# Kernel tuning notes

Hardware: AMD Instinct MI355X
Metric: run time of the kernel (lower is better)

Reference implementation:

```python
import jax, jax.numpy as jnp
import numpy as np

N_NODES = 50000
N_EDGES = 800000
EPS = 1e-12


def _l2norm(x):
    # F.normalize(x, p=2, dim=1)
    n = jnp.sqrt(jnp.sum(x * x, axis=1, keepdims=True))
    return x / jnp.maximum(n, EPS)


def _sage_layer(h, src, dst, inv_deg, W_self, W_neigh, b, last):
    # mean aggregation over in-neighbors: gather src feats, scatter-add to dst
    msg = jax.ops.segment_sum(h[src], dst, num_segments=N_NODES)  # [N, d]
    h_neigh = msg * inv_deg  # [N, d]
    rst = h @ W_self + h_neigh @ W_neigh + b
    if not last:
        rst = jax.nn.relu(rst)
        rst = _l2norm(rst)
    return rst


def setup_inputs() -> dict:
    key = jax.random.key(0)
    ks = jax.random.split(key, 10)
    d_in, d_h, d_out = 128, 128, 64
    s = lambda k, sh, fan: jax.random.normal(k, sh, jnp.float32) / np.sqrt(fan)
    return {
        "features": jax.random.normal(ks[0], (N_NODES, d_in), jnp.float32),
        "src": jax.random.randint(ks[1], (N_EDGES,), 0, N_NODES, jnp.int32),
        "dst": jax.random.randint(ks[2], (N_EDGES,), 0, N_NODES, jnp.int32),
        "W_self0": s(ks[3], (d_in, d_h), d_in),
        "W_neigh0": s(ks[4], (d_in, d_h), d_in),
        "b0": jnp.zeros((d_h,), jnp.float32),
        "W_self1": s(ks[5], (d_h, d_h), d_h),
        "W_neigh1": s(ks[6], (d_h, d_h), d_h),
        "b1": jnp.zeros((d_h,), jnp.float32),
        "W_self2": s(ks[7], (d_h, d_out), d_h),
        "W_neigh2": s(ks[8], (d_h, d_out), d_h),
        "b2": jnp.zeros((d_out,), jnp.float32),
    }


def reference(features, src, dst, W_self0, W_neigh0, b0, W_self1, W_neigh1, b1, W_self2, W_neigh2, b2):
    # in-degree for mean aggregation (clamped to avoid div-by-zero)
    deg = jax.ops.segment_sum(jnp.ones((N_EDGES,), jnp.float32), dst, num_segments=N_NODES)
    inv_deg = (1.0 / jnp.maximum(deg, 1.0))[:, None]  # [N,1]
    h = _sage_layer(features, src, dst, inv_deg, W_self0, W_neigh0, b0, last=False)
    h = _sage_layer(h, src, dst, inv_deg, W_self1, W_neigh1, b1, last=False)
    out = _sage_layer(h, src, dst, inv_deg, W_self2, W_neigh2, b2, last=True)
    return out
```

## Files before the change

kernel.cpp:

```cpp
#include <hip/hip_runtime.h>
#include <hip/hip_bf16.h>

#define N_NODES 50000
#define N_EDGES 800000
#define NBUCKET 196
#define NPB 256
#define BUCKET_CAP 7168
#define PART_EDGES 4096
#define PART_BLOCKS ((N_EDGES + PART_EDGES - 1) / PART_EDGES)
#define SENTINEL 0xFFFFFFFFu

typedef __attribute__((ext_vector_type(8))) short bf16x8;
typedef __attribute__((ext_vector_type(4))) float f32x4;

__device__ __forceinline__ float bf2f(unsigned short u) {
    unsigned int x = ((unsigned int)u) << 16;
    return __uint_as_float(x);
}
__device__ __forceinline__ unsigned short f2bf(float f) {
    unsigned int x = __float_as_uint(f);
    unsigned int lsb = (x >> 16) & 1u;
    x += 0x7fffu + lsb;
    return (unsigned short)(x >> 16);
}

#define NF2 ((N_NODES * 64 + 255) / 256)
__global__ __launch_bounds__(256) void k_prep(
        const float* __restrict__ Ws0, const float* __restrict__ Wn0,
        const float* __restrict__ Ws1, const float* __restrict__ Wn1,
        const float* __restrict__ Ws2, const float* __restrict__ Wn2,
        __hip_bfloat16* __restrict__ frag0, __hip_bfloat16* __restrict__ frag1,
        __hip_bfloat16* __restrict__ frag2,
        const float2* __restrict__ fin, unsigned int* __restrict__ fout,
        int* __restrict__ cursor, int* __restrict__ valid) {
    int b = blockIdx.x;
    if (b >= 40 + NF2) {
        int tid = threadIdx.x;
        if (tid < NBUCKET) { cursor[tid] = 0; valid[tid] = 0; }
        return;
    }
    if (b >= 40) {
        int i = (b - 40) * 256 + threadIdx.x;
        if (i < N_NODES * 64) {
            float2 v = fin[i];
            fout[i] = ((unsigned int)f2bf(v.y) << 16) | (unsigned int)f2bf(v.x);
        }
        return;
    }
    const float* Wself;
    const float* Wneigh;
    __hip_bfloat16* frag;
    int Dout, lb;
    if (b < 16)      { Wself = Ws0; Wneigh = Wn0; frag = frag0; Dout = 128; lb = b; }
    else if (b < 32) { Wself = Ws1; Wneigh = Wn1; frag = frag1; Dout = 128; lb = b - 16; }
    else             { Wself = Ws2; Wneigh = Wn2; frag = frag2; Dout = 64;  lb = b - 32; }
    int t = lb * 256 + threadIdx.x;
    int nCt = Dout >> 4;
    int total = nCt * 8 * 64;
    if (t >= total) return;
    int lane = t & 63;
    int kt = (t >> 6) & 7;
    int ct = t >> 9;
    int q = lane >> 4;
    int n = ct * 16 + (lane & 15);
    unsigned short* dstp = (unsigned short*)frag + ((size_t)((ct * 8 + kt) * 64 + lane)) * 8;
    #pragma unroll
    for (int j = 0; j < 8; ++j) {
        int k = kt * 32 + q * 8 + j;
        float v = (k < 128) ? Wself[k * Dout + n] : Wneigh[(k - 128) * Dout + n];
        dstp[j] = f2bf(v);
    }
}

__global__ __launch_bounds__(256) void k_partA(const int* __restrict__ src,
                                               const int* __restrict__ dst,
                                               int* __restrict__ cursor,
                                               int* __restrict__ valid,
                                               unsigned int* __restrict__ bucketArr) {
    __shared__ int hist[NBUCKET];
    __shared__ int base[NBUCKET];
    __shared__ int cnt[NBUCKET];
    int tid = threadIdx.x;
    if (tid < NBUCKET) hist[tid] = 0;
    __syncthreads();
    int e0 = blockIdx.x * PART_EDGES;
    for (int j = 0; j < PART_EDGES; j += 256) {
        int e = e0 + j + tid;
        if (e < N_EDGES) atomicAdd(&hist[dst[e] >> 8], 1);
    }
    __syncthreads();
    if (tid < NBUCKET) {
        int h = hist[tid];
        int hp = (h + 15) & ~15;
        int b0 = atomicAdd(&cursor[tid], hp);
        atomicAdd(&valid[tid], h);
        base[tid] = b0;
        cnt[tid] = 0;
        for (int k = h; k < hp; ++k) {
            int p = b0 + k;
            if (p < BUCKET_CAP) bucketArr[(size_t)tid * BUCKET_CAP + p] = SENTINEL;
        }
    }
    __syncthreads();
    for (int j = 0; j < PART_EDGES; j += 256) {
        int e = e0 + j + tid;
        if (e < N_EDGES) {
            int d = dst[e];
            int b = d >> 8;
            int p = base[b] + atomicAdd(&cnt[b], 1);
            if (p < BUCKET_CAP)
                bucketArr[(size_t)b * BUCKET_CAP + p] =
                    (unsigned int)src[e] | ((unsigned int)(d & 255) << 16);
        }
    }
}

__global__ __launch_bounds__(256) void k_scanB(const int* __restrict__ valid,
                                               int* __restrict__ gbase) {
    __shared__ int buf[256];
    int tid = threadIdx.x;
    int v = (tid < NBUCKET) ? valid[tid] : 0;
    int pv = (v + 15) & ~15;
    buf[tid] = pv;
    __syncthreads();
    for (int off = 1; off < 256; off <<= 1) {
        int t = (tid >= off) ? buf[tid - off] : 0;
        __syncthreads();
        buf[tid] += t;
        __syncthreads();
    }
    if (tid < NBUCKET) gbase[tid] = buf[tid] - pv;
}

__global__ __launch_bounds__(256) void k_partB(const unsigned int* __restrict__ bucketArr,
                                               const int* __restrict__ cursor,
                                               const int* __restrict__ gbase,
                                               int* __restrict__ off_beg,
                                               int* __restrict__ off_end,
                                               float* __restrict__ inv_deg,
                                               int* __restrict__ edge_src) {
    __shared__ unsigned int ed[BUCKET_CAP];
    __shared__ int csr[BUCKET_CAP];
    __shared__ int hist[256];
    __shared__ int lbase[256];
    __shared__ int lcnt[256];
    __shared__ int tot_s;
    int b = blockIdx.x;
    int tid = threadIdx.x;
    int size = min(cursor[b], BUCKET_CAP);
    int gb = gbase[b];
    int nbase = b * NPB;
    int ncount = min(NPB, N_NODES - nbase);
    hist[tid] = 0;
    __syncthreads();
    for (int j = 0; j < BUCKET_CAP; j += 256) {
        int i = j + tid;
        if (i < size) {
            unsigned int u = bucketArr[(size_t)b * BUCKET_CAP + i];
            ed[i] = u;
            if ((u >> 16) < 256u) atomicAdd(&hist[u >> 16], 1);
        }
    }
    __syncthreads();
    int v = hist[tid];
    lbase[tid] = v;
    __syncthreads();
    for (int off = 1; off < 256; off <<= 1) {
        int t = (tid >= off) ? lbase[tid - off] : 0;
        __syncthreads();
        lbase[tid] += t;
        __syncthreads();
    }
    int excl = lbase[tid] - v;
    if (tid == 255) tot_s = lbase[255];
    __syncthreads();
    lbase[tid] = excl;
    lcnt[tid] = 0;
    if (tid < ncount) {
        off_beg[nbase + tid] = gb + excl;
        off_end[nbase + tid] = gb + excl + v;
        inv_deg[nbase + tid] = 1.0f / (float)max(v, 1);
    }
    __syncthreads();
    for (int j = 0; j < BUCKET_CAP; j += 256) {
        int i = j + tid;
        if (i < size) {
            unsigned int u = ed[i];
            unsigned int ld = u >> 16;
            if (ld < 256u) {
                int p = lbase[ld] + atomicAdd(&lcnt[ld], 1);
                csr[p] = (int)(u & 0xffffu);
            }
        }
    }
    __syncthreads();
    int tot = tot_s;
    for (int j = 0; j < BUCKET_CAP; j += 256) {
        int i = j + tid;
        if (i < tot) edge_src[gb + i] = csr[i];
    }
}

__global__ void k_agg(const __hip_bfloat16* __restrict__ hv,
                      const int* __restrict__ off_beg, const int* __restrict__ off_end,
                      const int* __restrict__ edge_src, const float* __restrict__ inv_deg,
                      __hip_bfloat16* __restrict__ msg) {
    int gid = blockIdx.x * blockDim.x + threadIdx.x;
    int node = gid >> 6;
    int lane = gid & 63;
    if (node >= N_NODES) return;
    int half = lane >> 5;
    int sub = lane & 31;
    int beg = off_beg[node], end = off_end[node];
    const uint2* hp = (const uint2*)hv;

    float acc[4][4];
    #pragma unroll
    for (int g = 0; g < 4; ++g)
        #pragma unroll
        for (int c = 0; c < 4; ++c) acc[g][c] = 0.f;

    int i = beg;
    for (; i + 16 <= end; i += 16) {
        int s0 = edge_src[i + half];
        int s1 = edge_src[i + 2 + half];
        int s2 = edge_src[i + 4 + half];
        int s3 = edge_src[i + 6 + half];
        int s4 = edge_src[i + 8 + half];
        int s5 = edge_src[i + 10 + half];
        int s6 = edge_src[i + 12 + half];
        int s7 = edge_src[i + 14 + half];
        uint2 u0 = hp[(size_t)s0 * 32 + sub];
        uint2 u1 = hp[(size_t)s1 * 32 + sub];
        uint2 u2 = hp[(size_t)s2 * 32 + sub];
        uint2 u3 = hp[(size_t)s3 * 32 + sub];
        uint2 u4 = hp[(size_t)s4 * 32 + sub];
        uint2 u5 = hp[(size_t)s5 * 32 + sub];
        uint2 u6 = hp[(size_t)s6 * 32 + sub];
        uint2 u7 = hp[(size_t)s7 * 32 + sub];
        acc[0][0] += bf2f((unsigned short)(u0.x & 0xffffu)); acc[0][1] += bf2f((unsigned short)(u0.x >> 16));
        acc[0][2] += bf2f((unsigned short)(u0.y & 0xffffu)); acc[0][3] += bf2f((unsigned short)(u0.y >> 16));
        acc[1][0] += bf2f((unsigned short)(u1.x & 0xffffu)); acc[1][1] += bf2f((unsigned short)(u1.x >> 16));
        acc[1][2] += bf2f((unsigned short)(u1.y & 0xffffu)); acc[1][3] += bf2f((unsigned short)(u1.y >> 16));
        acc[2][0] += bf2f((unsigned short)(u2.x & 0xffffu)); acc[2][1] += bf2f((unsigned short)(u2.x >> 16));
        acc[2][2] += bf2f((unsigned short)(u2.y & 0xffffu)); acc[2][3] += bf2f((unsigned short)(u2.y >> 16));
        acc[3][0] += bf2f((unsigned short)(u3.x & 0xffffu)); acc[3][1] += bf2f((unsigned short)(u3.x >> 16));
        acc[3][2] += bf2f((unsigned short)(u3.y & 0xffffu)); acc[3][3] += bf2f((unsigned short)(u3.y >> 16));
        acc[0][0] += bf2f((unsigned short)(u4.x & 0xffffu)); acc[0][1] += bf2f((unsigned short)(u4.x >> 16));
        acc[0][2] += bf2f((unsigned short)(u4.y & 0xffffu)); acc[0][3] += bf2f((unsigned short)(u4.y >> 16));
        acc[1][0] += bf2f((unsigned short)(u5.x & 0xffffu)); acc[1][1] += bf2f((unsigned short)(u5.x >> 16));
        acc[1][2] += bf2f((unsigned short)(u5.y & 0xffffu)); acc[1][3] += bf2f((unsigned short)(u5.y >> 16));
        acc[2][0] += bf2f((unsigned short)(u6.x & 0xffffu)); acc[2][1] += bf2f((unsigned short)(u6.x >> 16));
        acc[2][2] += bf2f((unsigned short)(u6.y & 0xffffu)); acc[2][3] += bf2f((unsigned short)(u6.y >> 16));
        acc[3][0] += bf2f((unsigned short)(u7.x & 0xffffu)); acc[3][1] += bf2f((unsigned short)(u7.x >> 16));
        acc[3][2] += bf2f((unsigned short)(u7.y & 0xffffu)); acc[3][3] += bf2f((unsigned short)(u7.y >> 16));
    }
    for (; i + 8 <= end; i += 8) {
        int s0 = edge_src[i + half];
        int s1 = edge_src[i + 2 + half];
        int s2 = edge_src[i + 4 + half];
        int s3 = edge_src[i + 6 + half];
        uint2 u0 = hp[(size_t)s0 * 32 + sub];
        uint2 u1 = hp[(size_t)s1 * 32 + sub];
        uint2 u2 = hp[(size_t)s2 * 32 + sub];
        uint2 u3 = hp[(size_t)s3 * 32 + sub];
        acc[0][0] += bf2f((unsigned short)(u0.x & 0xffffu)); acc[0][1] += bf2f((unsigned short)(u0.x >> 16));
        acc[0][2] += bf2f((unsigned short)(u0.y & 0xffffu)); acc[0][3] += bf2f((unsigned short)(u0.y >> 16));
        acc[1][0] += bf2f((unsigned short)(u1.x & 0xffffu)); acc[1][1] += bf2f((unsigned short)(u1.x >> 16));
        acc[1][2] += bf2f((unsigned short)(u1.y & 0xffffu)); acc[1][3] += bf2f((unsigned short)(u1.y >> 16));
        acc[2][0] += bf2f((unsigned short)(u2.x & 0xffffu)); acc[2][1] += bf2f((unsigned short)(u2.x >> 16));
        acc[2][2] += bf2f((unsigned short)(u2.y & 0xffffu)); acc[2][3] += bf2f((unsigned short)(u2.y >> 16));
        acc[3][0] += bf2f((unsigned short)(u3.x & 0xffffu)); acc[3][1] += bf2f((unsigned short)(u3.x >> 16));
        acc[3][2] += bf2f((unsigned short)(u3.y & 0xffffu)); acc[3][3] += bf2f((unsigned short)(u3.y >> 16));
    }
    for (; i + 4 <= end; i += 4) {
        int s0 = edge_src[i + half];
        int s1 = edge_src[i + 2 + half];
        uint2 u0 = hp[(size_t)s0 * 32 + sub];
        uint2 u1 = hp[(size_t)s1 * 32 + sub];
        acc[0][0] += bf2f((unsigned short)(u0.x & 0xffffu)); acc[0][1] += bf2f((unsigned short)(u0.x >> 16));
        acc[0][2] += bf2f((unsigned short)(u0.y & 0xffffu)); acc[0][3] += bf2f((unsigned short)(u0.y >> 16));
        acc[1][0] += bf2f((unsigned short)(u1.x & 0xffffu)); acc[1][1] += bf2f((unsigned short)(u1.x >> 16));
        acc[1][2] += bf2f((unsigned short)(u1.y & 0xffffu)); acc[1][3] += bf2f((unsigned short)(u1.y >> 16));
    }
    for (; i + 2 <= end; i += 2) {
        int s0 = edge_src[i + half];
        uint2 u0 = hp[(size_t)s0 * 32 + sub];
        acc[0][0] += bf2f((unsigned short)(u0.x & 0xffffu)); acc[0][1] += bf2f((unsigned short)(u0.x >> 16));
        acc[0][2] += bf2f((unsigned short)(u0.y & 0xffffu)); acc[0][3] += bf2f((unsigned short)(u0.y >> 16));
    }
    if (i < end && half == 0) {
        int s0 = edge_src[i];
        uint2 u0 = hp[(size_t)s0 * 32 + sub];
        acc[0][0] += bf2f((unsigned short)(u0.x & 0xffffu)); acc[0][1] += bf2f((unsigned short)(u0.x >> 16));
        acc[0][2] += bf2f((unsigned short)(u0.y & 0xffffu)); acc[0][3] += bf2f((unsigned short)(u0.y >> 16));
    }

    float r0 = acc[0][0] + acc[1][0] + acc[2][0] + acc[3][0];
    float r1 = acc[0][1] + acc[1][1] + acc[2][1] + acc[3][1];
    float r2 = acc[0][2] + acc[1][2] + acc[2][2] + acc[3][2];
    float r3 = acc[0][3] + acc[1][3] + acc[2][3] + acc[3][3];
    r0 += __shfl_xor(r0, 32);
    r1 += __shfl_xor(r1, 32);
    r2 += __shfl_xor(r2, 32);
    r3 += __shfl_xor(r3, 32);
    if (half == 0) {
        float w = inv_deg[node];
        uint2 o;
        o.x = ((unsigned int)f2bf(r1 * w) << 16) | (unsigned int)f2bf(r0 * w);
        o.y = ((unsigned int)f2bf(r3 * w) << 16) | (unsigned int)f2bf(r2 * w);
        ((uint2*)msg)[(size_t)node * 32 + sub] = o;
    }
}

template <int NCT, bool LAST>
__global__ __launch_bounds__(256) void k_gemm(const __hip_bfloat16* __restrict__ Aself,
                                              const __hip_bfloat16* __restrict__ Aneigh,
                                              const __hip_bfloat16* __restrict__ frag,
                                              const float* __restrict__ bias,
                                              void* __restrict__ out_) {
    constexpr int Dout = NCT * 16;
    int tid = threadIdx.x;
    int wv = tid >> 6, lane = tid & 63;
    int n0 = blockIdx.x * 64 + wv * 16;
    if (n0 >= N_NODES) return;
    int q = lane >> 4, l15 = lane & 15;
    int rowA = n0 + l15;
    if (rowA > N_NODES - 1) rowA = N_NODES - 1;

    f32x4 acc[NCT];
    #pragma unroll
    for (int c = 0; c < NCT; ++c) acc[c] = (f32x4){0.f, 0.f, 0.f, 0.f};

    const bf16x8* fragv = (const bf16x8*)frag;
    #pragma unroll
    for (int kt = 0; kt < 8; ++kt) {
        int kb = (kt & 3) * 32 + q * 8;
        const __hip_bfloat16* Ab = (kt < 4) ? Aself : Aneigh;
        bf16x8 a = *(const bf16x8*)(Ab + (size_t)rowA * 128 + kb);
        #pragma unroll
        for (int ct = 0; ct < NCT; ++ct) {
            bf16x8 b = fragv[(ct * 8 + kt) * 64 + lane];
            acc[ct] = __builtin_amdgcn_mfma_f32_16x16x32_bf16(a, b, acc[ct], 0, 0, 0);
        }
    }

    float ss[4] = {0.f, 0.f, 0.f, 0.f};
    #pragma unroll
    for (int ct = 0; ct < NCT; ++ct) {
        float bc = bias[ct * 16 + l15];
        #pragma unroll
        for (int r = 0; r < 4; ++r) {
            float v = acc[ct][r] + bc;
            if (!LAST) v = fmaxf(v, 0.0f);
            acc[ct][r] = v;
            ss[r] += v * v;
        }
    }

    float scale[4];
    #pragma unroll
    for (int r = 0; r < 4; ++r) {
        if (!LAST) {
            float s = ss[r];
            s += __shfl_xor(s, 1);
            s += __shfl_xor(s, 2);
            s += __shfl_xor(s, 4);
            s += __shfl_xor(s, 8);
            scale[r] = 1.0f / fmaxf(sqrtf(s), 1e-12f);
        } else {
            scale[r] = 1.0f;
        }
    }

    #pragma unroll
    for (int ct = 0; ct < NCT; ++ct) {
        #pragma unroll
        for (int r = 0; r < 4; ++r) {
            int row = n0 + q * 4 + r;
            if (row < N_NODES) {
                float v = acc[ct][r] * scale[r];
                if (LAST)
                    ((float*)out_)[(size_t)row * Dout + ct * 16 + l15] = v;
                else
                    ((unsigned short*)out_)[(size_t)row * Dout + ct * 16 + l15] = f2bf(v);
            }
        }
    }
}


extern "C" void kernel_launch(void* const* d_in, const int* in_sizes, int n_in,
                              void* d_out, int out_size, void* d_ws, size_t ws_size,
                              hipStream_t stream) {
    const float* features = (const float*)d_in[0];
    const int* src = (const int*)d_in[1];
    const int* dst = (const int*)d_in[2];
    const float* Ws0 = (const float*)d_in[3];
    const float* Wn0 = (const float*)d_in[4];
    const float* b0  = (const float*)d_in[5];
    const float* Ws1 = (const float*)d_in[6];
    const float* Wn1 = (const float*)d_in[7];
    const float* b1  = (const float*)d_in[8];
    const float* Ws2 = (const float*)d_in[9];
    const float* Wn2 = (const float*)d_in[10];
    const float* b2  = (const float*)d_in[11];
    float* out = (float*)d_out;

    char* ws = (char*)d_ws;
    size_t off = 0;
    auto alloc = [&](size_t bytes) -> void* {
        void* p = ws + off;
        off = (off + bytes + 255) & ~(size_t)255;
        return p;
    };
    int*   cursor   = (int*)alloc((size_t)NBUCKET * 4);
    int*   valid    = (int*)alloc((size_t)NBUCKET * 4);
    int*   gbase    = (int*)alloc((size_t)NBUCKET * 4);
    unsigned int* bucketArr = (unsigned int*)alloc((size_t)NBUCKET * BUCKET_CAP * 4);
    int*   off_beg  = (int*)alloc((size_t)N_NODES * 4);
    int*   off_end  = (int*)alloc((size_t)N_NODES * 4);
    int*   edge_src = (int*)alloc((size_t)(N_EDGES + NBUCKET * 16) * 4);
    float* inv_deg  = (float*)alloc((size_t)N_NODES * 4);
    __hip_bfloat16* fbf = (__hip_bfloat16*)alloc((size_t)N_NODES * 128 * 2);
    __hip_bfloat16* msg = (__hip_bfloat16*)alloc((size_t)N_NODES * 128 * 2);
    __hip_bfloat16* h1  = (__hip_bfloat16*)alloc((size_t)N_NODES * 128 * 2);
    __hip_bfloat16* h2  = (__hip_bfloat16*)alloc((size_t)N_NODES * 128 * 2);
    __hip_bfloat16* frag0 = (__hip_bfloat16*)alloc((size_t)8 * 8 * 64 * 8 * 2);
    __hip_bfloat16* frag1 = (__hip_bfloat16*)alloc((size_t)8 * 8 * 64 * 8 * 2);
    __hip_bfloat16* frag2 = (__hip_bfloat16*)alloc((size_t)4 * 8 * 64 * 8 * 2);

    k_prep<<<40 + NF2 + 1, 256, 0, stream>>>(Ws0, Wn0, Ws1, Wn1, Ws2, Wn2,
                                             frag0, frag1, frag2,
                                             (const float2*)features, (unsigned int*)fbf,
                                             cursor, valid);
    k_partA<<<PART_BLOCKS, 256, 0, stream>>>(src, dst, cursor, valid, bucketArr);
    k_scanB<<<1, 256, 0, stream>>>(valid, gbase);
    k_partB<<<NBUCKET, 256, 0, stream>>>(bucketArr, cursor, gbase,
                                         off_beg, off_end, inv_deg, edge_src);

    const int aggGrid = (N_NODES * 64) / 256;
    const int gemmGrid = (N_NODES + 63) / 64;

    k_agg<<<aggGrid, 256, 0, stream>>>(fbf, off_beg, off_end, edge_src, inv_deg, msg);
    k_gemm<8, false><<<gemmGrid, 256, 0, stream>>>(fbf, msg, frag0, b0, h1);
    k_agg<<<aggGrid, 256, 0, stream>>>(h1, off_beg, off_end, edge_src, inv_deg, msg);
    k_gemm<8, false><<<gemmGrid, 256, 0, stream>>>(h1, msg, frag1, b1, h2);
    k_agg<<<aggGrid, 256, 0, stream>>>(h2, off_beg, off_end, edge_src, inv_deg, msg);
    k_gemm<4, true><<<gemmGrid, 256, 0, stream>>>(h2, msg, frag2, b2, out);
}
```

Measured before the change: 267.7 us.

## Fuse neighbor aggregation into per-layer GEMM kernel via LDS message tile

```diff
diff --git a/kernel.cpp b/kernel.cpp
--- a/kernel.cpp
+++ b/kernel.cpp
@@ -201,147 +201,115 @@
     }
 }
 
-__global__ void k_agg(const __hip_bfloat16* __restrict__ hv,
-                      const int* __restrict__ off_beg, const int* __restrict__ off_end,
-                      const int* __restrict__ edge_src, const float* __restrict__ inv_deg,
-                      __hip_bfloat16* __restrict__ msg) {
-    int gid = blockIdx.x * blockDim.x + threadIdx.x;
-    int node = gid >> 6;
-    int lane = gid & 63;
-    if (node >= N_NODES) return;
-    int half = lane >> 5;
-    int sub = lane & 31;
-    int beg = off_beg[node], end = off_end[node];
-    const uint2* hp = (const uint2*)hv;
-
-    float acc[4][4];
-    #pragma unroll
-    for (int g = 0; g < 4; ++g)
-        #pragma unroll
-        for (int c = 0; c < 4; ++c) acc[g][c] = 0.f;
-
-    int i = beg;
-    for (; i + 16 <= end; i += 16) {
-        int s0 = edge_src[i + half];
-        int s1 = edge_src[i + 2 + half];
-        int s2 = edge_src[i + 4 + half];
-        int s3 = edge_src[i + 6 + half];
-        int s4 = edge_src[i + 8 + half];
-        int s5 = edge_src[i + 10 + half];
-        int s6 = edge_src[i + 12 + half];
-        int s7 = edge_src[i + 14 + half];
-        uint2 u0 = hp[(size_t)s0 * 32 + sub];
-        uint2 u1 = hp[(size_t)s1 * 32 + sub];
-        uint2 u2 = hp[(size_t)s2 * 32 + sub];
-        uint2 u3 = hp[(size_t)s3 * 32 + sub];
-        uint2 u4 = hp[(size_t)s4 * 32 + sub];
-        uint2 u5 = hp[(size_t)s5 * 32 + sub];
-        uint2 u6 = hp[(size_t)s6 * 32 + sub];
-        uint2 u7 = hp[(size_t)s7 * 32 + sub];
-        acc[0][0] += bf2f((unsigned short)(u0.x & 0xffffu)); acc[0][1] += bf2f((unsigned short)(u0.x >> 16));
-        acc[0][2] += bf2f((unsigned short)(u0.y & 0xffffu)); acc[0][3] += bf2f((unsigned short)(u0.y >> 16));
-        acc[1][0] += bf2f((unsigned short)(u1.x & 0xffffu)); acc[1][1] += bf2f((unsigned short)(u1.x >> 16));
-        acc[1][2] += bf2f((unsigned short)(u1.y & 0xffffu)); acc[1][3] += bf2f((unsigned short)(u1.y >> 16));
-        acc[2][0] += bf2f((unsigned short)(u2.x & 0xffffu)); acc[2][1] += bf2f((unsigned short)(u2.x >> 16));
-        acc[2][2] += bf2f((unsigned short)(u2.y & 0xffffu)); acc[2][3] += bf2f((unsigned short)(u2.y >> 16));
-        acc[3][0] += bf2f((unsigned short)(u3.x & 0xffffu)); acc[3][1] += bf2f((unsigned short)(u3.x >> 16));
-        acc[3][2] += bf2f((unsigned short)(u3.y & 0xffffu)); acc[3][3] += bf2f((unsigned short)(u3.y >> 16));
-        acc[0][0] += bf2f((unsigned short)(u4.x & 0xffffu)); acc[0][1] += bf2f((unsigned short)(u4.x >> 16));
-        acc[0][2] += bf2f((unsigned short)(u4.y & 0xffffu)); acc[0][3] += bf2f((unsigned short)(u4.y >> 16));
-        acc[1][0] += bf2f((unsigned short)(u5.x & 0xffffu)); acc[1][1] += bf2f((unsigned short)(u5.x >> 16));
-        acc[1][2] += bf2f((unsigned short)(u5.y & 0xffffu)); acc[1][3] += bf2f((unsigned short)(u5.y >> 16));
-        acc[2][0] += bf2f((unsigned short)(u6.x & 0xffffu)); acc[2][1] += bf2f((unsigned short)(u6.x >> 16));
-        acc[2][2] += bf2f((unsigned short)(u6.y & 0xffffu)); acc[2][3] += bf2f((unsigned short)(u6.y >> 16));
-        acc[3][0] += bf2f((unsigned short)(u7.x & 0xffffu)); acc[3][1] += bf2f((unsigned short)(u7.x >> 16));
-        acc[3][2] += bf2f((unsigned short)(u7.y & 0xffffu)); acc[3][3] += bf2f((unsigned short)(u7.y >> 16));
-    }
-    for (; i + 8 <= end; i += 8) {
-        int s0 = edge_src[i + half];
-        int s1 = edge_src[i + 2 + half];
-        int s2 = edge_src[i + 4 + half];
-        int s3 = edge_src[i + 6 + half];
-        uint2 u0 = hp[(size_t)s0 * 32 + sub];
-        uint2 u1 = hp[(size_t)s1 * 32 + sub];
-        uint2 u2 = hp[(size_t)s2 * 32 + sub];
-        uint2 u3 = hp[(size_t)s3 * 32 + sub];
-        acc[0][0] += bf2f((unsigned short)(u0.x & 0xffffu)); acc[0][1] += bf2f((unsigned short)(u0.x >> 16));
-        acc[0][2] += bf2f((unsigned short)(u0.y & 0xffffu)); acc[0][3] += bf2f((unsigned short)(u0.y >> 16));
-        acc[1][0] += bf2f((unsigned short)(u1.x & 0xffffu)); acc[1][1] += bf2f((unsigned short)(u1.x >> 16));
-        acc[1][2] += bf2f((unsigned short)(u1.y & 0xffffu)); acc[1][3] += bf2f((unsigned short)(u1.y >> 16));
-        acc[2][0] += bf2f((unsigned short)(u2.x & 0xffffu)); acc[2][1] += bf2f((unsigned short)(u2.x >> 16));
-        acc[2][2] += bf2f((unsigned short)(u2.y & 0xffffu)); acc[2][3] += bf2f((unsigned short)(u2.y >> 16));
-        acc[3][0] += bf2f((unsigned short)(u3.x & 0xffffu)); acc[3][1] += bf2f((unsigned short)(u3.x >> 16));
-        acc[3][2] += bf2f((unsigned short)(u3.y & 0xffffu)); acc[3][3] += bf2f((unsigned short)(u3.y >> 16));
-    }
-    for (; i + 4 <= end; i += 4) {
-        int s0 = edge_src[i + half];
-        int s1 = edge_src[i + 2 + half];
-        uint2 u0 = hp[(size_t)s0 * 32 + sub];
-        uint2 u1 = hp[(size_t)s1 * 32 + sub];
-        acc[0][0] += bf2f((unsigned short)(u0.x & 0xffffu)); acc[0][1] += bf2f((unsigned short)(u0.x >> 16));
-        acc[0][2] += bf2f((unsigned short)(u0.y & 0xffffu)); acc[0][3] += bf2f((unsigned short)(u0.y >> 16));
-        acc[1][0] += bf2f((unsigned short)(u1.x & 0xffffu)); acc[1][1] += bf2f((unsigned short)(u1.x >> 16));
-        acc[1][2] += bf2f((unsigned short)(u1.y & 0xffffu)); acc[1][3] += bf2f((unsigned short)(u1.y >> 16));
-    }
-    for (; i + 2 <= end; i += 2) {
-        int s0 = edge_src[i + half];
-        uint2 u0 = hp[(size_t)s0 * 32 + sub];
-        acc[0][0] += bf2f((unsigned short)(u0.x & 0xffffu)); acc[0][1] += bf2f((unsigned short)(u0.x >> 16));
-        acc[0][2] += bf2f((unsigned short)(u0.y & 0xffffu)); acc[0][3] += bf2f((unsigned short)(u0.y >> 16));
-    }
-    if (i < end && half == 0) {
-        int s0 = edge_src[i];
-        uint2 u0 = hp[(size_t)s0 * 32 + sub];
-        acc[0][0] += bf2f((unsigned short)(u0.x & 0xffffu)); acc[0][1] += bf2f((unsigned short)(u0.x >> 16));
-        acc[0][2] += bf2f((unsigned short)(u0.y & 0xffffu)); acc[0][3] += bf2f((unsigned short)(u0.y >> 16));
-    }
-
-    float r0 = acc[0][0] + acc[1][0] + acc[2][0] + acc[3][0];
-    float r1 = acc[0][1] + acc[1][1] + acc[2][1] + acc[3][1];
-    float r2 = acc[0][2] + acc[1][2] + acc[2][2] + acc[3][2];
-    float r3 = acc[0][3] + acc[1][3] + acc[2][3] + acc[3][3];
-    r0 += __shfl_xor(r0, 32);
-    r1 += __shfl_xor(r1, 32);
-    r2 += __shfl_xor(r2, 32);
-    r3 += __shfl_xor(r3, 32);
-    if (half == 0) {
-        float w = inv_deg[node];
-        uint2 o;
-        o.x = ((unsigned int)f2bf(r1 * w) << 16) | (unsigned int)f2bf(r0 * w);
-        o.y = ((unsigned int)f2bf(r3 * w) << 16) | (unsigned int)f2bf(r2 * w);
-        ((uint2*)msg)[(size_t)node * 32 + sub] = o;
-    }
-}
-
 template <int NCT, bool LAST>
-__global__ __launch_bounds__(256) void k_gemm(const __hip_bfloat16* __restrict__ Aself,
-                                              const __hip_bfloat16* __restrict__ Aneigh,
-                                              const __hip_bfloat16* __restrict__ frag,
-                                              const float* __restrict__ bias,
-                                              void* __restrict__ out_) {
+__global__ __launch_bounds__(256) void k_fused(
+        const __hip_bfloat16* __restrict__ hv,
+        const int* __restrict__ off_beg, const int* __restrict__ off_end,
+        const int* __restrict__ edge_src, const float* __restrict__ inv_deg,
+        const __hip_bfloat16* __restrict__ frag, const float* __restrict__ bias,
+        void* __restrict__ out_) {
     constexpr int Dout = NCT * 16;
+    constexpr int P = 136;
+    __shared__ short lmsg[64 * P];
     int tid = threadIdx.x;
     int wv = tid >> 6, lane = tid & 63;
-    int n0 = blockIdx.x * 64 + wv * 16;
-    if (n0 >= N_NODES) return;
+    int half = lane >> 5, sub = lane & 31;
+    int nblk = blockIdx.x * 64;
+    const uint2* hp = (const uint2*)hv;
+
+    for (int t = 0; t < 16; ++t) {
+        int nloc = wv * 16 + t;
+        int node = nblk + nloc;
+        float acc[4][4];
+        #pragma unroll
+        for (int g = 0; g < 4; ++g)
+            #pragma unroll
+            for (int c = 0; c < 4; ++c) acc[g][c] = 0.f;
+        if (node < N_NODES) {
+            int beg = off_beg[node], end = off_end[node];
+            int i = beg;
+            for (; i + 8 <= end; i += 8) {
+                int s0 = edge_src[i + half];
+                int s1 = edge_src[i + 2 + half];
+                int s2 = edge_src[i + 4 + half];
+                int s3 = edge_src[i + 6 + half];
+                uint2 u0 = hp[(size_t)s0 * 32 + sub];
+                uint2 u1 = hp[(size_t)s1 * 32 + sub];
+                uint2 u2 = hp[(size_t)s2 * 32 + sub];
+                uint2 u3 = hp[(size_t)s3 * 32 + sub];
+                acc[0][0] += bf2f((unsigned short)(u0.x & 0xffffu)); acc[0][1] += bf2f((unsigned short)(u0.x >> 16));
+                acc[0][2] += bf2f((unsigned short)(u0.y & 0xffffu)); acc[0][3] += bf2f((unsigned short)(u0.y >> 16));
+                acc[1][0] += bf2f((unsigned short)(u1.x & 0xffffu)); acc[1][1] += bf2f((unsigned short)(u1.x >> 16));
+                acc[1][2] += bf2f((unsigned short)(u1.y & 0xffffu)); acc[1][3] += bf2f((unsigned short)(u1.y >> 16));
+                acc[2][0] += bf2f((unsigned short)(u2.x & 0xffffu)); acc[2][1] += bf2f((unsigned short)(u2.x >> 16));
+                acc[2][2] += bf2f((unsigned short)(u2.y & 0xffffu)); acc[2][3] += bf2f((unsigned short)(u2.y >> 16));
+                acc[3][0] += bf2f((unsigned short)(u3.x & 0xffffu)); acc[3][1] += bf2f((unsigned short)(u3.x >> 16));
+                acc[3][2] += bf2f((unsigned short)(u3.y & 0xffffu)); acc[3][3] += bf2f((unsigned short)(u3.y >> 16));
+            }
+            for (; i + 4 <= end; i += 4) {
+                int s0 = edge_src[i + half];
+                int s1 = edge_src[i + 2 + half];
+                uint2 u0 = hp[(size_t)s0 * 32 + sub];
+                uint2 u1 = hp[(size_t)s1 * 32 + sub];
+                acc[0][0] += bf2f((unsigned short)(u0.x & 0xffffu)); acc[0][1] += bf2f((unsigned short)(u0.x >> 16));
+                acc[0][2] += bf2f((unsigned short)(u0.y & 0xffffu)); acc[0][3] += bf2f((unsigned short)(u0.y >> 16));
+                acc[1][0] += bf2f((unsigned short)(u1.x & 0xffffu)); acc[1][1] += bf2f((unsigned short)(u1.x >> 16));
+                acc[1][2] += bf2f((unsigned short)(u1.y & 0xffffu)); acc[1][3] += bf2f((unsigned short)(u1.y >> 16));
+            }
+            for (; i + 2 <= end; i += 2) {
+                int s0 = edge_src[i + half];
+                uint2 u0 = hp[(size_t)s0 * 32 + sub];
+                acc[0][0] += bf2f((unsigned short)(u0.x & 0xffffu)); acc[0][1] += bf2f((unsigned short)(u0.x >> 16));
+                acc[0][2] += bf2f((unsigned short)(u0.y & 0xffffu)); acc[0][3] += bf2f((unsigned short)(u0.y >> 16));
+            }
+            if (i < end && half == 0) {
+                int s0 = edge_src[i];
+                uint2 u0 = hp[(size_t)s0 * 32 + sub];
+                acc[0][0] += bf2f((unsigned short)(u0.x & 0xffffu)); acc[0][1] += bf2f((unsigned short)(u0.x >> 16));
+                acc[0][2] += bf2f((unsigned short)(u0.y & 0xffffu)); acc[0][3] += bf2f((unsigned short)(u0.y >> 16));
+            }
+        }
+        float r0 = acc[0][0] + acc[1][0] + acc[2][0] + acc[3][0];
+        float r1 = acc[0][1] + acc[1][1] + acc[2][1] + acc[3][1];
+        float r2 = acc[0][2] + acc[1][2] + acc[2][2] + acc[3][2];
+        float r3 = acc[0][3] + acc[1][3] + acc[2][3] + acc[3][3];
+        r0 += __shfl_xor(r0, 32);
+        r1 += __shfl_xor(r1, 32);
+        r2 += __shfl_xor(r2, 32);
+        r3 += __shfl_xor(r3, 32);
+        if (half == 0) {
+            float w = (node < N_NODES) ? inv_deg[node] : 0.0f;
+            uint2 o;
+            o.x = ((unsigned int)f2bf(r1 * w) << 16) | (unsigned int)f2bf(r0 * w);
+            o.y = ((unsigned int)f2bf(r3 * w) << 16) | (unsigned int)f2bf(r2 * w);
+            *(uint2*)&lmsg[nloc * P + 4 * sub] = o;
+        }
+    }
+    __syncthreads();
+
     int q = lane >> 4, l15 = lane & 15;
+    int n0 = nblk + wv * 16;
     int rowA = n0 + l15;
     if (rowA > N_NODES - 1) rowA = N_NODES - 1;
 
-    f32x4 acc[NCT];
-    #pragma unroll
-    for (int c = 0; c < NCT; ++c) acc[c] = (f32x4){0.f, 0.f, 0.f, 0.f};
+    f32x4 gacc[NCT];
+    #pragma unroll
+    for (int c = 0; c < NCT; ++c) gacc[c] = (f32x4){0.f, 0.f, 0.f, 0.f};
 
     const bf16x8* fragv = (const bf16x8*)frag;
     #pragma unroll
     for (int kt = 0; kt < 8; ++kt) {
         int kb = (kt & 3) * 32 + q * 8;
-        const __hip_bfloat16* Ab = (kt < 4) ? Aself : Aneigh;
-        bf16x8 a = *(const bf16x8*)(Ab + (size_t)rowA * 128 + kb);
+        bf16x8 a;
+        if (kt < 4) {
+            a = *(const bf16x8*)(hv + (size_t)rowA * 128 + kb);
+        } else {
+            a = *(const bf16x8*)&lmsg[(wv * 16 + l15) * P + kb];
+        }
         #pragma unroll
         for (int ct = 0; ct < NCT; ++ct) {
             bf16x8 b = fragv[(ct * 8 + kt) * 64 + lane];
-            acc[ct] = __builtin_amdgcn_mfma_f32_16x16x32_bf16(a, b, acc[ct], 0, 0, 0);
+            gacc[ct] = __builtin_amdgcn_mfma_f32_16x16x32_bf16(a, b, gacc[ct], 0, 0, 0);
         }
     }
 
@@ -351,9 +319,9 @@
         float bc = bias[ct * 16 + l15];
         #pragma unroll
         for (int r = 0; r < 4; ++r) {
-            float v = acc[ct][r] + bc;
+            float v = gacc[ct][r] + bc;
             if (!LAST) v = fmaxf(v, 0.0f);
-            acc[ct][r] = v;
+            gacc[ct][r] = v;
             ss[r] += v * v;
         }
     }
@@ -379,7 +347,7 @@
         for (int r = 0; r < 4; ++r) {
             int row = n0 + q * 4 + r;
             if (row < N_NODES) {
-                float v = acc[ct][r] * scale[r];
+                float v = gacc[ct][r] * scale[r];
                 if (LAST)
                     ((float*)out_)[(size_t)row * Dout + ct * 16 + l15] = v;
                 else
@@ -423,7 +391,6 @@
     int*   edge_src = (int*)alloc((size_t)(N_EDGES + NBUCKET * 16) * 4);
     float* inv_deg  = (float*)alloc((size_t)N_NODES * 4);
     __hip_bfloat16* fbf = (__hip_bfloat16*)alloc((size_t)N_NODES * 128 * 2);
-    __hip_bfloat16* msg = (__hip_bfloat16*)alloc((size_t)N_NODES * 128 * 2);
     __hip_bfloat16* h1  = (__hip_bfloat16*)alloc((size_t)N_NODES * 128 * 2);
     __hip_bfloat16* h2  = (__hip_bfloat16*)alloc((size_t)N_NODES * 128 * 2);
     __hip_bfloat16* frag0 = (__hip_bfloat16*)alloc((size_t)8 * 8 * 64 * 8 * 2);
@@ -439,13 +406,12 @@
     k_partB<<<NBUCKET, 256, 0, stream>>>(bucketArr, cursor, gbase,
                                          off_beg, off_end, inv_deg, edge_src);
 
-    const int aggGrid = (N_NODES * 64) / 256;
-    const int gemmGrid = (N_NODES + 63) / 64;
-
-    k_agg<<<aggGrid, 256, 0, stream>>>(fbf, off_beg, off_end, edge_src, inv_deg, msg);
-    k_gemm<8, false><<<gemmGrid, 256, 0, stream>>>(fbf, msg, frag0, b0, h1);
-    k_agg<<<aggGrid, 256, 0, stream>>>(h1, off_beg, off_end, edge_src, inv_deg, msg);
-    k_gemm<8, false><<<gemmGrid, 256, 0, stream>>>(h1, msg, frag1, b1, h2);
-    k_agg<<<aggGrid, 256, 0, stream>>>(h2, off_beg, off_end, edge_src, inv_deg, msg);
-    k_gemm<4, true><<<gemmGrid, 256, 0, stream>>>(h2, msg, frag2, b2, out);
-}
+    const int fusedGrid = (N_NODES + 63) / 64;
+
+    k_fused<8, false><<<fusedGrid, 256, 0, stream>>>(fbf, off_beg, off_end, edge_src,
+                                                     inv_deg, frag0, b0, h1);
+    k_fused<8, false><<<fusedGrid, 256, 0, stream>>>(h1, off_beg, off_end, edge_src,
+                                                     inv_deg, frag1, b1, h2);
+    k_fused<4, true><<<fusedGrid, 256, 0, stream>>>(h2, off_beg, off_end, edge_src,
+                                                    inv_deg, frag2, b2, out);
+}
```

After: 390.4 us. 45.8% more time.
